# Kernel optimization log

Hardware: AMD Instinct MI355X
Metric: run time of the kernel (lower is better)

## Reference

```python
import jax, jax.numpy as jnp
import numpy as np

B, S, D = 2, 2048, 2048
NH, NKV, HD = 16, 4, 128
EPS = 1e-6


def rmsnorm(x, w, eps=EPS):
    # torch.nn.RMSNorm: x * rsqrt(mean(x^2) + eps) * weight
    ms = jnp.mean(jnp.square(x), axis=-1, keepdims=True)
    return x * jax.lax.rsqrt(ms + eps) * w


def apply_rotary_emb(x, freqs_cis):
    # x: (B, S, H, HD); freqs_cis: (S, HD//2, 2) -> pairwise complex rotation (gpt-fast style)
    xs = x.reshape(*x.shape[:-1], -1, 2)          # (B,S,H,HD//2,2)
    fc = freqs_cis[None, :, None, :, :]           # (1,S,1,HD//2,2)
    xr, xi = xs[..., 0], xs[..., 1]
    fr, fi = fc[..., 0], fc[..., 1]
    out = jnp.stack([xr * fr - xi * fi, xi * fr + xr * fi], axis=-1)
    return out.reshape(x.shape)


def setup_inputs() -> dict:
    key = jax.random.key(0)
    ks = jax.random.split(key, 4)
    x = jax.random.normal(ks[0], (B, S, D), dtype=jnp.float32)
    freqs_cis = jax.random.normal(ks[1], (S, HD // 2, 2), dtype=jnp.float32)
    wqkv = jax.random.normal(ks[2], ((NH + 2 * NKV) * HD, D), dtype=jnp.float32) * (D ** -0.5)
    wo = jax.random.normal(ks[3], (NH * HD, D), dtype=jnp.float32).T * ((NH * HD) ** -0.5)
    wo = jnp.asarray(wo)  # (D, NH*HD) torch layout (out,in)
    q_norm_w = jnp.ones((HD,), dtype=jnp.float32)
    k_norm_w = jnp.ones((HD,), dtype=jnp.float32)
    return {"x": x, "freqs_cis": freqs_cis, "wqkv": wqkv, "wo": wo,
            "q_norm_w": q_norm_w, "k_norm_w": k_norm_w}


def reference(x, freqs_cis, wqkv, wo, q_norm_w, k_norm_w):
    b, s, _ = x.shape
    q_size, kv_size = NH * HD, NKV * HD
    qkv = jnp.einsum('bsd,ed->bse', x, wqkv)  # fused QKV projection
    q, k, v = jnp.split(qkv, [q_size, q_size + kv_size], axis=-1)
    q = q.reshape(b, s, NH, HD)
    k = k.reshape(b, s, NKV, HD)
    v = v.reshape(b, s, NKV, HD)
    q = rmsnorm(q, q_norm_w)
    k = rmsnorm(k, k_norm_w)
    q = apply_rotary_emb(q, freqs_cis)
    k = apply_rotary_emb(k, freqs_cis)
    # GQA: repeat_interleave KV heads to NH
    rep = NH // NKV
    k = jnp.repeat(k, rep, axis=2)  # (b,s,NH,HD)
    v = jnp.repeat(v, rep, axis=2)
    scale = 1.0 / np.sqrt(HD)
    scores = jnp.einsum('bqhd,bkhd->bhqk', q, k) * scale
    causal = jnp.tril(jnp.ones((s, s), dtype=bool))
    scores = jnp.where(causal[None, None], scores, -jnp.inf)
    attn = jax.nn.softmax(scores, axis=-1)
    y = jnp.einsum('bhqk,bkhd->bqhd', attn, v)
    y = y.reshape(b, s, q_size)
    return jnp.einsum('bse,de->bsd', y, wo)
```

## Files before the change

kernel.cpp:

```cpp
#include <hip/hip_runtime.h>
#include <math.h>

constexpr int B_ = 2, S_ = 2048, D_ = 2048, NH_ = 16, NKV_ = 4, HD_ = 128;
constexpr int EQKV_ = (NH_ + 2 * NKV_) * HD_;
constexpr int M_ = B_ * S_;
constexpr float EPS_ = 1e-6f;
constexpr float QSCALE_ = 0.08838834764831845f;

typedef __attribute__((ext_vector_type(8))) short bf16x8;
typedef __attribute__((ext_vector_type(4))) float f32x4;
typedef __attribute__((address_space(1))) unsigned int gu32;
typedef __attribute__((address_space(3))) unsigned int lu32;

__device__ inline ushort f2bf(float f) {
    unsigned u = __float_as_uint(f);
    return (ushort)((u + 0x7FFF + ((u >> 16) & 1)) >> 16);
}

__global__ __launch_bounds__(256) void pack_bf16(
    const float* __restrict__ in, ushort* __restrict__ out, int n4)
{
    int i = blockIdx.x * 256 + threadIdx.x;
    if (i >= n4) return;
    float4 f = ((const float4*)in)[i];
    ushort4 u;
    u.x = f2bf(f.x); u.y = f2bf(f.y); u.z = f2bf(f.z); u.w = f2bf(f.w);
    ((ushort4*)out)[i] = u;
}

__global__ __launch_bounds__(256) void gemm_nt_bf16(
    const ushort* __restrict__ A, const ushort* __restrict__ W,
    float* __restrict__ C, int M, int N, int K)
{
    __shared__ ushort As[128 * 32];
    __shared__ ushort Bs[128 * 32];
    const int t = threadIdx.x;
    const int wave = t >> 6, lane = t & 63;
    const int m0 = blockIdx.y * 128, n0 = blockIdx.x * 128;
    const int wm = (wave >> 1) * 64, wn = (wave & 1) * 64;
    const int lrow = lane & 15, lquad = lane >> 4;

    f32x4 acc[4][4];
#pragma unroll
    for (int i = 0; i < 4; ++i)
#pragma unroll
        for (int j = 0; j < 4; ++j) acc[i][j] = (f32x4){0.f, 0.f, 0.f, 0.f};

    for (int k0 = 0; k0 < K; k0 += 32) {
        __syncthreads();
#pragma unroll
        for (int i = 0; i < 2; ++i) {
            int chunk = t + 256 * i;
            int row = chunk >> 2, seg = chunk & 3;
            int ubase = (wave * 64 + 256 * i) * 8;
            __builtin_amdgcn_global_load_lds(
                (const gu32*)(A + (size_t)(m0 + row) * K + k0 + seg * 8),
                (lu32*)(As + ubase), 16, 0, 0);
            __builtin_amdgcn_global_load_lds(
                (const gu32*)(W + (size_t)(n0 + row) * K + k0 + seg * 8),
                (lu32*)(Bs + ubase), 16, 0, 0);
        }
        __syncthreads();

        bf16x8 af[4], bf[4];
#pragma unroll
        for (int i = 0; i < 4; ++i) {
            af[i] = *(const bf16x8*)(As + (wm + i * 16 + lrow) * 32 + lquad * 8);
            bf[i] = *(const bf16x8*)(Bs + (wn + i * 16 + lrow) * 32 + lquad * 8);
        }
#pragma unroll
        for (int i = 0; i < 4; ++i)
#pragma unroll
            for (int j = 0; j < 4; ++j)
                acc[i][j] = __builtin_amdgcn_mfma_f32_16x16x32_bf16(
                    af[i], bf[j], acc[i][j], 0, 0, 0);
    }
#pragma unroll
    for (int i = 0; i < 4; ++i)
#pragma unroll
        for (int j = 0; j < 4; ++j) {
            float* cp = C + (size_t)(m0 + wm + i * 16 + lquad * 4) * N
                          + n0 + wn + j * 16 + lrow;
#pragma unroll
            for (int r = 0; r < 4; ++r) cp[(size_t)r * N] = acc[i][j][r];
        }
}

__global__ __launch_bounds__(256) void gemm_qkv_fused(
    const ushort* __restrict__ A,
    const ushort* __restrict__ W,
    const float* __restrict__ freqs,
    const float* __restrict__ qw, const float* __restrict__ kw,
    ushort* __restrict__ qo, ushort* __restrict__ ko, ushort* __restrict__ vo,
    int K)
{
    __shared__ __align__(16) ushort smem[128 * 136];
    __shared__ float rsbuf[256];
    ushort* As = smem;
    ushort* Bs = smem + 4096;
    ushort* Lt = smem;

    const int t = threadIdx.x;
    const int wave = t >> 6, lane = t & 63;
    const int m0 = blockIdx.y * 128, n0 = blockIdx.x * 128;
    const int wm = (wave >> 1) * 64, wn = (wave & 1) * 64;
    const int half = wave & 1;
    const int lrow = lane & 15, lquad = lane >> 4;
    const int head = n0 >> 7;
    const int b = m0 >> 11, s0 = m0 & (S_ - 1);

    f32x4 acc[4][4];
#pragma unroll
    for (int i = 0; i < 4; ++i)
#pragma unroll
        for (int j = 0; j < 4; ++j) acc[i][j] = (f32x4){0.f, 0.f, 0.f, 0.f};

    for (int k0 = 0; k0 < K; k0 += 32) {
        __syncthreads();
#pragma unroll
        for (int i = 0; i < 2; ++i) {
            int chunk = t + 256 * i;
            int row = chunk >> 2, seg = chunk & 3;
            int ubase = (wave * 64 + 256 * i) * 8;
            __builtin_amdgcn_global_load_lds(
                (const gu32*)(A + (size_t)(m0 + row) * K + k0 + seg * 8),
                (lu32*)(As + ubase), 16, 0, 0);
            __builtin_amdgcn_global_load_lds(
                (const gu32*)(W + (size_t)(n0 + row) * K + k0 + seg * 8),
                (lu32*)(Bs + ubase), 16, 0, 0);
        }
        __syncthreads();

        bf16x8 af[4], bf[4];
#pragma unroll
        for (int i = 0; i < 4; ++i) {
            af[i] = *(const bf16x8*)(As + (wm + i * 16 + lrow) * 32 + lquad * 8);
            bf[i] = *(const bf16x8*)(Bs + (wn + i * 16 + lrow) * 32 + lquad * 8);
        }
#pragma unroll
        for (int i = 0; i < 4; ++i)
#pragma unroll
            for (int j = 0; j < 4; ++j)
                acc[i][j] = __builtin_amdgcn_mfma_f32_16x16x32_bf16(
                    af[i], bf[j], acc[i][j], 0, 0, 0);
    }
    __syncthreads();

    float part[4][4];
    if (head < NH_ + NKV_) {
#pragma unroll
        for (int i = 0; i < 4; ++i)
#pragma unroll
            for (int r = 0; r < 4; ++r) {
                float p = acc[i][0][r] * acc[i][0][r]
                        + acc[i][1][r] * acc[i][1][r]
                        + acc[i][2][r] * acc[i][2][r]
                        + acc[i][3][r] * acc[i][3][r];
#pragma unroll
                for (int off = 1; off < 16; off <<= 1) p += __shfl_xor(p, off);
                part[i][r] = p;
                if (lrow == 0)
                    rsbuf[half * 128 + wm + i * 16 + lquad * 4 + r] = p;
            }
    }
    __syncthreads();

    if (head < NH_ + NKV_) {
        const float* nw = (head < NH_) ? qw : kw;
        float wv[4];
#pragma unroll
        for (int j = 0; j < 4; ++j) wv[j] = nw[wn + j * 16 + lrow];
#pragma unroll
        for (int i = 0; i < 4; ++i)
#pragma unroll
            for (int r = 0; r < 4; ++r) {
                const int rowid = wm + i * 16 + lquad * 4 + r;
                const int s = s0 + rowid;
                const float total = part[i][r] + rsbuf[(half ^ 1) * 128 + rowid];
                const float rs = rsqrtf(total * (1.0f / HD_) + EPS_);
#pragma unroll
                for (int j = 0; j < 4; ++j) {
                    const int d = wn + j * 16 + lrow;
                    const float xn = acc[i][j][r] * rs * wv[j];
                    const float other = __shfl_xor(xn, 1);
                    const float fr = freqs[s * HD_ + (d & ~1)];
                    const float fi = freqs[s * HD_ + (d & ~1) + 1];
                    float out = (d & 1) ? fmaf(xn, fr, other * fi)
                                        : fmaf(xn, fr, -other * fi);
                    if (head < NH_) out *= QSCALE_;
                    Lt[rowid * 136 + d] = f2bf(out);
                }
            }
    } else {
#pragma unroll
        for (int i = 0; i < 4; ++i)
#pragma unroll
            for (int j = 0; j < 4; ++j)
#pragma unroll
                for (int r = 0; r < 4; ++r)
                    Lt[(wn + j * 16 + lrow) * 136 + wm + i * 16 + lquad * 4 + r]
                        = f2bf(acc[i][j][r]);
    }
    __syncthreads();

    const int g = t >> 4, lx16 = t & 15;
    if (head < NH_) {
        ushort* dst0 = qo + ((size_t)(b * NH_ + head) * S_ + s0) * HD_;
#pragma unroll
        for (int it = 0; it < 8; ++it) {
            const int rowid = it * 16 + g;
            uint4 v = *(const uint4*)(Lt + rowid * 136 + lx16 * 8);
            *(uint4*)(dst0 + (size_t)rowid * HD_ + lx16 * 8) = v;
        }
    } else if (head < NH_ + NKV_) {
        const int kh = head - NH_;
        ushort* dst0 = ko + ((size_t)(b * NKV_ + kh) * S_ + s0) * HD_;
#pragma unroll
        for (int it = 0; it < 8; ++it) {
            const int rowid = it * 16 + g;
            uint4 v = *(const uint4*)(Lt + rowid * 136 + lx16 * 8);
            *(uint4*)(dst0 + (size_t)rowid * HD_ + lx16 * 8) = v;
        }
    } else {
        const int vh = head - (NH_ + NKV_);
        ushort* dst0 = vo + ((size_t)(b * NKV_ + vh) * HD_) * S_ + s0;
#pragma unroll
        for (int it = 0; it < 8; ++it) {
            const int rowid = it * 16 + g;
            uint4 v = *(const uint4*)(Lt + rowid * 136 + lx16 * 8);
            *(uint4*)(dst0 + (size_t)rowid * S_ + lx16 * 8) = v;
        }
    }
}

__global__ __launch_bounds__(256, 3) void flash_attn_mfma(
    const ushort* __restrict__ Q,
    const ushort* __restrict__ K,
    const ushort* __restrict__ V,
    ushort* __restrict__ Y)
{
    __shared__ __align__(16) ushort Ks[4 * 64 * 32];
    __shared__ __align__(16) ushort Vs[2 * 128 * 32];
    __shared__ __align__(16) ushort Ps[4 * 16 * 72];

    const int t = threadIdx.x, w = t >> 6, lane = t & 63;
    const int lx = lane & 15, quad = lane >> 4;
    const int h = blockIdx.y, b = blockIdx.z;
    const int qt = (int)gridDim.x - 1 - (int)blockIdx.x;
    const int q0 = qt * 64;
    const int kvh = h >> 2;
    const int srow = lane >> 2, sseg = lane & 3;
    const int wslot = (sseg ^ ((srow >> 1) & 3)) * 8;
    const int rslot = (quad ^ ((lx >> 1) & 3)) * 8;

    const ushort* qb = Q + ((size_t)(b * NH_ + h) * S_ + q0) * HD_;
    const ushort* ksrc = K + ((size_t)(b * NKV_ + kvh) * S_ + w * 16 + srow) * HD_
                           + sseg * 8;
    const ushort* vb = V + ((size_t)(b * NKV_ + kvh) * HD_) * S_;
    const ushort* vsrc0 = vb + (size_t)(w * 16 + srow) * S_ + sseg * 8;
    const ushort* vsrc1 = vb + (size_t)(64 + w * 16 + srow) * S_ + sseg * 8;
    ushort* kdst = Ks + w * 512 + srow * 32 + wslot;
    ushort* vdst0 = Vs + (w * 16 + srow) * 32 + wslot;
    ushort* vdst1 = Vs + (64 + w * 16 + srow) * 32 + wslot;

    bf16x8 aq[4];
#pragma unroll
    for (int ks = 0; ks < 4; ++ks)
        aq[ks] = *(const bf16x8*)(qb + (size_t)(w * 16 + lx) * HD_ + ks * 32 + quad * 8);

    f32x4 o[8];
#pragma unroll
    for (int j = 0; j < 8; ++j) o[j] = (f32x4){0.f, 0.f, 0.f, 0.f};
    float mrow[4] = {-INFINITY, -INFINITY, -INFINITY, -INFINITY};
    float lp[4] = {0.f, 0.f, 0.f, 0.f};

    uint4 kr0, kr1, kr2, kr3, vr0, vr1, vr2, vr3;
    kr0 = *(const uint4*)(ksrc +  0);
    kr1 = *(const uint4*)(ksrc + 32);
    kr2 = *(const uint4*)(ksrc + 64);
    kr3 = *(const uint4*)(ksrc + 96);
    vr0 = *(const uint4*)(vsrc0 +  0);
    vr1 = *(const uint4*)(vsrc1 +  0);
    vr2 = *(const uint4*)(vsrc0 + 32);
    vr3 = *(const uint4*)(vsrc1 + 32);

    const int ntiles = qt + 1;
    for (int tk = 0; tk < ntiles; ++tk) {
        const int k0 = tk * 64;
        asm volatile("s_barrier" ::: "memory");
        *(uint4*)(kdst +    0) = kr0;
        *(uint4*)(kdst + 2048) = kr1;
        *(uint4*)(kdst + 4096) = kr2;
        *(uint4*)(kdst + 6144) = kr3;
        *(uint4*)(vdst0 +    0) = vr0;
        *(uint4*)(vdst1 +    0) = vr1;
        *(uint4*)(vdst0 + 4096) = vr2;
        *(uint4*)(vdst1 + 4096) = vr3;
        asm volatile("s_waitcnt lgkmcnt(0)" ::: "memory");
        asm volatile("s_barrier" ::: "memory");

        if (tk + 1 < ntiles) {
            const size_t ko8 = (size_t)(k0 + 64);
            kr0 = *(const uint4*)(ksrc + ko8 * HD_ +  0);
            kr1 = *(const uint4*)(ksrc + ko8 * HD_ + 32);
            kr2 = *(const uint4*)(ksrc + ko8 * HD_ + 64);
            kr3 = *(const uint4*)(ksrc + ko8 * HD_ + 96);
            vr0 = *(const uint4*)(vsrc0 + ko8 +  0);
            vr1 = *(const uint4*)(vsrc1 + ko8 +  0);
            vr2 = *(const uint4*)(vsrc0 + ko8 + 32);
            vr3 = *(const uint4*)(vsrc1 + ko8 + 32);
        }

        f32x4 s[4];
#pragma unroll
        for (int j = 0; j < 4; ++j) s[j] = (f32x4){0.f, 0.f, 0.f, 0.f};
        __builtin_amdgcn_s_setprio(1);
#pragma unroll
        for (int ks = 0; ks < 4; ++ks) {
#pragma unroll
            for (int j = 0; j < 4; ++j) {
                bf16x8 bk = *(const bf16x8*)(Ks + ks * 2048 + (j * 16 + lx) * 32 + rslot);
                s[j] = __builtin_amdgcn_mfma_f32_16x16x32_bf16(aq[ks], bk, s[j], 0, 0, 0);
            }
        }
        __builtin_amdgcn_s_setprio(0);

        const int qrow_base = q0 + w * 16 + quad * 4;
        if (tk == ntiles - 1) {
#pragma unroll
            for (int reg = 0; reg < 4; ++reg) {
                const int qrow = qrow_base + reg;
#pragma unroll
                for (int j = 0; j < 4; ++j)
                    if (k0 + lx + 16 * j > qrow) s[j][reg] = -INFINITY;
            }
        }

        float rmx[4];
        bool need = false;
#pragma unroll
        for (int reg = 0; reg < 4; ++reg) {
            rmx[reg] = fmaxf(fmaxf(s[0][reg], s[1][reg]),
                             fmaxf(s[2][reg], s[3][reg]));
            need |= (rmx[reg] > mrow[reg] + 8.0f);
        }
        if (__any(need)) {
#pragma unroll
            for (int reg = 0; reg < 4; ++reg) {
                float rm = rmx[reg];
#pragma unroll
                for (int off = 1; off < 16; off <<= 1)
                    rm = fmaxf(rm, __shfl_xor(rm, off));
                const float mn = fmaxf(mrow[reg], rm);
                const float alpha = __expf(mrow[reg] - mn);
                mrow[reg] = mn;
                lp[reg] *= alpha;
#pragma unroll
                for (int j = 0; j < 8; ++j) o[j][reg] *= alpha;
            }
        }
#pragma unroll
        for (int reg = 0; reg < 4; ++reg) {
#pragma unroll
            for (int j = 0; j < 4; ++j) {
                const float p = __expf(s[j][reg] - mrow[reg]);
                lp[reg] += p;
                Ps[w * 1152 + (quad * 4 + reg) * 72 + lx + 16 * j] = f2bf(p);
            }
        }

        bf16x8 ap[2];
#pragma unroll
        for (int ks2 = 0; ks2 < 2; ++ks2)
            ap[ks2] = *(const bf16x8*)(Ps + w * 1152 + lx * 72 + ks2 * 32 + quad * 8);
        __builtin_amdgcn_s_setprio(1);
#pragma unroll
        for (int jd = 0; jd < 8; ++jd) {
#pragma unroll
            for (int ks2 = 0; ks2 < 2; ++ks2) {
                bf16x8 bv = *(const bf16x8*)(Vs + ks2 * 4096 + (jd * 16 + lx) * 32 + rslot);
                o[jd] = __builtin_amdgcn_mfma_f32_16x16x32_bf16(ap[ks2], bv, o[jd], 0, 0, 0);
            }
        }
        __builtin_amdgcn_s_setprio(0);
    }

#pragma unroll
    for (int reg = 0; reg < 4; ++reg) {
        float l = lp[reg];
#pragma unroll
        for (int off = 1; off < 16; off <<= 1) l += __shfl_xor(l, off);
        const float inv = 1.0f / l;
        const size_t yb = (size_t)(b * S_ + q0 + w * 16 + quad * 4 + reg) * (NH_ * HD_)
                        + h * HD_ + lx;
#pragma unroll
        for (int jd = 0; jd < 8; ++jd)
            Y[yb + jd * 16] = f2bf(o[jd][reg] * inv);
    }
}

extern "C" void kernel_launch(void* const* d_in, const int* in_sizes, int n_in,
                              void* d_out, int out_size, void* d_ws, size_t ws_size,
                              hipStream_t stream)
{
    const float* x     = (const float*)d_in[0];
    const float* freqs = (const float*)d_in[1];
    const float* wqkv  = (const float*)d_in[2];
    const float* wo    = (const float*)d_in[3];
    const float* qw    = (const float*)d_in[4];
    const float* kw    = (const float*)d_in[5];
    float* out = (float*)d_out;

    char* ws = (char*)d_ws;
    ushort* qbf    = (ushort*)(ws + 0);
    ushort* kbf    = (ushort*)(ws + 16777216);
    ushort* vtb    = (ushort*)(ws + 20971520);
    ushort* ybf    = (ushort*)(ws + 25165824);
    ushort* wobf   = (ushort*)(ws + 41943040);
    ushort* wqkvbf = (ushort*)(ws + 50331648);
    ushort* xbf    = (ushort*)(ws + 83886080);

    pack_bf16<<<(M_ * D_ / 4 + 255) / 256, 256, 0, stream>>>(x, xbf, M_ * D_ / 4);
    pack_bf16<<<(EQKV_ * D_ / 4 + 255) / 256, 256, 0, stream>>>(wqkv, wqkvbf,
                                                                EQKV_ * D_ / 4);
    gemm_qkv_fused<<<dim3(EQKV_ / 128, M_ / 128), 256, 0, stream>>>(
        xbf, wqkvbf, freqs, qw, kw, qbf, kbf, vtb, D_);
    pack_bf16<<<(D_ * NH_ * HD_ / 4 + 255) / 256, 256, 0, stream>>>(
        wo, wobf, D_ * NH_ * HD_ / 4);
    flash_attn_mfma<<<dim3(S_ / 64, NH_, B_), 256, 0, stream>>>(qbf, kbf, vtb, ybf);
    gemm_nt_bf16<<<dim3(D_ / 128, M_ / 128), 256, 0, stream>>>(
        ybf, wobf, out, M_, D_, NH_ * HD_);
}
```

Baseline: 366.2 us.

## Split long causal query tiles across two blocks with a combine kernel

The upper 16 query tiles, which have the most key tiles under the causal mask, are each split into two blocks that process halves of the key range. Each half writes unnormalized fp32 partial outputs plus row max and sum to workspace. A new combine kernel merges the two halves with softmax rescaling. This is meant to balance work across blocks and shorten the tail, at the cost of an extra launch and extra fp32 traffic. The partials reuse workspace regions that earlier kernels have finished with.

```diff
diff --git a/kernel.cpp b/kernel.cpp
--- a/kernel.cpp
+++ b/kernel.cpp
@@ -237,7 +237,9 @@
     const ushort* __restrict__ Q,
     const ushort* __restrict__ K,
     const ushort* __restrict__ V,
-    ushort* __restrict__ Y)
+    ushort* __restrict__ Y,
+    float* __restrict__ OP,
+    float* __restrict__ ML)
 {
     __shared__ __align__(16) ushort Ks[4 * 64 * 32];
     __shared__ __align__(16) ushort Vs[2 * 128 * 32];
@@ -246,7 +248,24 @@
     const int t = threadIdx.x, w = t >> 6, lane = t & 63;
     const int lx = lane & 15, quad = lane >> 4;
     const int h = blockIdx.y, b = blockIdx.z;
-    const int qt = (int)gridDim.x - 1 - (int)blockIdx.x;
+
+    const int gx = blockIdx.x;
+    int qt, halfsel, tk0, tk1;
+    bool split;
+    if (gx < 32) {
+        split = true;
+        qt = 31 - (gx >> 1);
+        halfsel = gx & 1;
+        const int nt = qt + 1, nt0 = nt >> 1;
+        tk0 = halfsel ? nt0 : 0;
+        tk1 = halfsel ? nt : nt0;
+    } else {
+        split = false;
+        qt = 47 - gx;
+        halfsel = 0;
+        tk0 = 0;
+        tk1 = qt + 1;
+    }
     const int q0 = qt * 64;
     const int kvh = h >> 2;
     const int srow = lane >> 2, sseg = lane & 3;
@@ -275,17 +294,19 @@
     float lp[4] = {0.f, 0.f, 0.f, 0.f};
 
     uint4 kr0, kr1, kr2, kr3, vr0, vr1, vr2, vr3;
-    kr0 = *(const uint4*)(ksrc +  0);
-    kr1 = *(const uint4*)(ksrc + 32);
-    kr2 = *(const uint4*)(ksrc + 64);
-    kr3 = *(const uint4*)(ksrc + 96);
-    vr0 = *(const uint4*)(vsrc0 +  0);
-    vr1 = *(const uint4*)(vsrc1 +  0);
-    vr2 = *(const uint4*)(vsrc0 + 32);
-    vr3 = *(const uint4*)(vsrc1 + 32);
-
-    const int ntiles = qt + 1;
-    for (int tk = 0; tk < ntiles; ++tk) {
+    {
+        const size_t kb0 = (size_t)tk0 * 64;
+        kr0 = *(const uint4*)(ksrc + kb0 * HD_ +  0);
+        kr1 = *(const uint4*)(ksrc + kb0 * HD_ + 32);
+        kr2 = *(const uint4*)(ksrc + kb0 * HD_ + 64);
+        kr3 = *(const uint4*)(ksrc + kb0 * HD_ + 96);
+        vr0 = *(const uint4*)(vsrc0 + kb0 +  0);
+        vr1 = *(const uint4*)(vsrc1 + kb0 +  0);
+        vr2 = *(const uint4*)(vsrc0 + kb0 + 32);
+        vr3 = *(const uint4*)(vsrc1 + kb0 + 32);
+    }
+
+    for (int tk = tk0; tk < tk1; ++tk) {
         const int k0 = tk * 64;
         asm volatile("s_barrier" ::: "memory");
         *(uint4*)(kdst +    0) = kr0;
@@ -299,7 +320,7 @@
         asm volatile("s_waitcnt lgkmcnt(0)" ::: "memory");
         asm volatile("s_barrier" ::: "memory");
 
-        if (tk + 1 < ntiles) {
+        if (tk + 1 < tk1) {
             const size_t ko8 = (size_t)(k0 + 64);
             kr0 = *(const uint4*)(ksrc + ko8 * HD_ +  0);
             kr1 = *(const uint4*)(ksrc + ko8 * HD_ + 32);
@@ -326,7 +347,7 @@
         __builtin_amdgcn_s_setprio(0);
 
         const int qrow_base = q0 + w * 16 + quad * 4;
-        if (tk == ntiles - 1) {
+        if (tk == qt) {
 #pragma unroll
             for (int reg = 0; reg < 4; ++reg) {
                 const int qrow = qrow_base + reg;
@@ -390,12 +411,60 @@
         float l = lp[reg];
 #pragma unroll
         for (int off = 1; off < 16; off <<= 1) l += __shfl_xor(l, off);
-        const float inv = 1.0f / l;
-        const size_t yb = (size_t)(b * S_ + q0 + w * 16 + quad * 4 + reg) * (NH_ * HD_)
-                        + h * HD_ + lx;
-#pragma unroll
-        for (int jd = 0; jd < 8; ++jd)
-            Y[yb + jd * 16] = f2bf(o[jd][reg] * inv);
+        lp[reg] = l;
+    }
+    if (!split) {
+#pragma unroll
+        for (int reg = 0; reg < 4; ++reg) {
+            const float inv = 1.0f / lp[reg];
+            const size_t yb = (size_t)(b * S_ + q0 + w * 16 + quad * 4 + reg) * (NH_ * HD_)
+                            + h * HD_ + lx;
+#pragma unroll
+            for (int jd = 0; jd < 8; ++jd)
+                Y[yb + jd * 16] = f2bf(o[jd][reg] * inv);
+        }
+    } else {
+        const int bh = b * NH_ + h;
+        const int st = qt - 16;
+        const size_t pidx = (size_t)(bh * 16 + st) * 2 + halfsel;
+        float* mlb = ML + pidx * 128;
+#pragma unroll
+        for (int reg = 0; reg < 4; ++reg) {
+            const int row = w * 16 + quad * 4 + reg;
+            if (lx == 0) {
+                mlb[row] = mrow[reg];
+                mlb[64 + row] = lp[reg];
+            }
+            float* ob = OP + (pidx * 64 + row) * 128 + lx;
+#pragma unroll
+            for (int jd = 0; jd < 8; ++jd)
+                ob[jd * 16] = o[jd][reg];
+        }
+    }
+}
+
+__global__ __launch_bounds__(256) void attn_combine(
+    const float* __restrict__ OP, const float* __restrict__ ML,
+    ushort* __restrict__ Y)
+{
+    const int st = blockIdx.x, h = blockIdx.y, b = blockIdx.z;
+    const int bh = b * NH_ + h;
+    const int d = threadIdx.x & 127, rg = threadIdx.x >> 7;
+    const size_t p0 = (size_t)(bh * 16 + st) * 2;
+    const float* ml0 = ML + p0 * 128;
+    const float* ml1 = ML + (p0 + 1) * 128;
+    const float* o0 = OP + p0 * 64 * 128;
+    const float* o1 = OP + (p0 + 1) * 64 * 128;
+    const int q0 = (16 + st) * 64;
+#pragma unroll
+    for (int r = rg; r < 64; r += 2) {
+        const float m0 = ml0[r], l0 = ml0[64 + r];
+        const float m1 = ml1[r], l1 = ml1[64 + r];
+        const float m = fmaxf(m0, m1);
+        const float w0 = __expf(m0 - m), w1 = __expf(m1 - m);
+        const float inv = 1.0f / (l0 * w0 + l1 * w1);
+        const float v = (o0[r * 128 + d] * w0 + o1[r * 128 + d] * w1) * inv;
+        Y[((size_t)(b * S_ + q0 + r)) * (NH_ * HD_) + h * HD_ + d] = f2bf(v);
     }
 }
 
@@ -419,6 +488,8 @@
     ushort* wobf   = (ushort*)(ws + 41943040);
     ushort* wqkvbf = (ushort*)(ws + 50331648);
     ushort* xbf    = (ushort*)(ws + 83886080);
+    float*  OP     = (float*)(ws + 50331648);
+    float*  ML     = (float*)(ws + 83886080);
 
     pack_bf16<<<(M_ * D_ / 4 + 255) / 256, 256, 0, stream>>>(x, xbf, M_ * D_ / 4);
     pack_bf16<<<(EQKV_ * D_ / 4 + 255) / 256, 256, 0, stream>>>(wqkv, wqkvbf,
@@ -427,7 +498,9 @@
         xbf, wqkvbf, freqs, qw, kw, qbf, kbf, vtb, D_);
     pack_bf16<<<(D_ * NH_ * HD_ / 4 + 255) / 256, 256, 0, stream>>>(
         wo, wobf, D_ * NH_ * HD_ / 4);
-    flash_attn_mfma<<<dim3(S_ / 64, NH_, B_), 256, 0, stream>>>(qbf, kbf, vtb, ybf);
+    flash_attn_mfma<<<dim3(48, NH_, B_), 256, 0, stream>>>(qbf, kbf, vtb, ybf,
+                                                           OP, ML);
+    attn_combine<<<dim3(16, NH_, B_), 256, 0, stream>>>(OP, ML, ybf);
     gemm_nt_bf16<<<dim3(D_ / 128, M_ / 128), 256, 0, stream>>>(
         ybf, wobf, out, M_, D_, NH_ * HD_);
 }
```

Result: faster. 349.5 us (-4.6%).
